# Kernel tuning notes

Hardware: AMD Instinct MI355X
Metric: run time of the kernel (lower is better)

## Reference

```python
import jax, jax.numpy as jnp
import numpy as np

B, C, H, W = 4, 320, 32, 32
HEADS = 8
LTXT, DCROSS = 77, 768
HW = H * W


def _ln(x, w, b, eps=1e-5):
    mu = x.mean(-1, keepdims=True)
    var = jnp.var(x, axis=-1, keepdims=True)
    return (x - mu) * jax.lax.rsqrt(var + eps) * w + b


def _gn(x, w, b, groups=32, eps=1e-6):
    Bx, Cx, Hx, Wx = x.shape
    xg = x.reshape(Bx, groups, -1)
    mu = xg.mean(-1, keepdims=True)
    var = jnp.var(xg, axis=-1, keepdims=True)
    xn = ((xg - mu) * jax.lax.rsqrt(var + eps)).reshape(Bx, Cx, Hx, Wx)
    return xn * w[None, :, None, None] + b[None, :, None, None]


def _attn(q, k, v, bias=None):
    Bq, S, Cd = q.shape
    dh = Cd // HEADS
    qh = q.reshape(Bq, S, HEADS, dh)
    kh = k.reshape(Bq, -1, HEADS, dh)
    vh = v.reshape(Bq, -1, HEADS, dh)
    s = jnp.einsum('bqhd,bkhd->bhqk', qh, kh) * (1.0 / np.sqrt(dh))
    if bias is not None:
        s = s + bias  # additive 0/1 otsu mask, exactly as the torch code passes it
    p = jax.nn.softmax(s, axis=-1)
    o = jnp.einsum('bhqk,bkhd->bqhd', p, vh).reshape(Bq, S, Cd)
    return o, p


def _block(x, ctx, prm, bias=None):
    # BasicTransformerBlock: self-attn -> cross-attn (returns probs) -> GEGLU FF
    (ln1w, ln1b, qkv, ow, ob, ln2w, ln2b, q2, kv2, o2w, o2b,
     ln3w, ln3b, ff1w, ff1b, ff2w, ff2b) = prm
    h = _ln(x, ln1w, ln1b)
    q, k, v = jnp.split(h @ qkv, 3, axis=-1)
    o, _ = _attn(q, k, v)
    x = x + o @ ow + ob
    h = _ln(x, ln2w, ln2b)
    k2, v2 = jnp.split(ctx @ kv2, 2, axis=-1)
    o2, p2 = _attn(h @ q2, k2, v2, bias)
    x = x + o2 @ o2w + o2b
    h = _ln(x, ln3w, ln3b)
    a, g = jnp.split(h @ ff1w + ff1b, 2, axis=-1)
    x = x + (a * jax.nn.gelu(g)) @ ff2w + ff2b
    return x, p2


def _otsu(m):
    # vectorized version of the 10-threshold otsu loop (m: [B/2, N])
    mn = m.min(-1, keepdims=True)
    mx = m.max(-1, keepdims=True)
    x = (m - mn) / (mx - mn)
    n = x.shape[-1]
    ts = jnp.arange(10, dtype=x.dtype) * 0.1  # thresholds t*0.1
    low = x[:, None, :] < ts[None, :, None]   # [B/2, 10, N]
    cnt_low = low.sum(-1).astype(x.dtype)
    cnt_high = n - cnt_low
    sum_low = jnp.where(low, x[:, None, :], 0.0).sum(-1)
    sum_high = x.sum(-1, keepdims=True) - sum_low
    mu_low = jnp.where(cnt_low > 0, sum_low / jnp.maximum(cnt_low, 1.0), jnp.nan)
    mu_high = jnp.where(cnt_high > 0, sum_high / jnp.maximum(cnt_high, 1.0), jnp.nan)
    g = (cnt_low / n) * (cnt_high / n) * (mu_low - mu_high) ** 2
    g = jnp.where(jnp.isnan(g), -jnp.inf, g)  # torch: nan > max_g is False -> skipped
    best = jnp.argmax(g, axis=-1)             # first max == torch strict-> ties keep earliest
    gmax = jnp.take_along_axis(g, best[:, None], axis=-1)[:, 0]
    thr = jnp.where(gmax > 0, best.astype(x.dtype) * 0.1, 0.0)[:, None]
    return jnp.where(x < thr, 0.0, jnp.where(x > thr, 1.0, x))


def _fwd(gn_w, gn_b, pin_w, pin_b,
         b_ln1w, b_ln1b, b_qkv, b_ow, b_ob, b_ln2w, b_ln2b, b_q2, b_kv2, b_o2w, b_o2b,
         b_ln3w, b_ln3b, b_ff1w, b_ff1b, b_ff2w, b_ff2b,
         i_ln1w, i_ln1b, i_qkv, i_ow, i_ob, i_ln2w, i_ln2b, i_q2, i_kv2, i_o2w, i_o2b,
         i_ln3w, i_ln3b, i_ff1w, i_ff1b, i_ff2w, i_ff2b,
         pout_w, pout_b, hidden_states, encoder_hidden_states,
         ph_b, ph_t, eot_b, eot_t):
    residual = hidden_states
    h = _gn(hidden_states, gn_w, gn_b)
    h = h.transpose(0, 2, 3, 1).reshape(B, HW, C)
    h = h @ pin_w + pin_b  # use_linear_projection path
    blk = (b_ln1w, b_ln1b, b_qkv, b_ow, b_ob, b_ln2w, b_ln2b, b_q2, b_kv2, b_o2w, b_o2b,
           b_ln3w, b_ln3b, b_ff1w, b_ff1b, b_ff2w, b_ff2b)
    iblk = (i_ln1w, i_ln1b, i_qkv, i_ow, i_ob, i_ln2w, i_ln2b, i_q2, i_kv2, i_o2w, i_o2b,
            i_ln3w, i_ln3b, i_ff1w, i_ff1b, i_ff2w, i_ff2b)
    h, probs = _block(h, encoder_hidden_states, blk)   # probs [B, heads, HW, 77]
    ap = probs.mean(1)[B // 2:]                        # head-avg attn_probs, cond half
    attn = ap.transpose(0, 2, 1)                       # [B/2, 77, HW]
    attn_ph = attn[ph_b, ph_t]                         # [B/2, HW]
    attn_eot = jax.lax.stop_gradient(attn[eot_b, eot_t])
    loss_reg = jnp.mean((attn_ph / attn_ph.max(-1, keepdims=True)
                         - attn_eot / attn_eot.max(-1, keepdims=True)) ** 2)
    mask = _otsu(jax.lax.stop_gradient(attn_ph))       # [B/2, HW]
    bias = mask[:, None, None, :]                      # broadcast over heads and queries
    hs, img = h[:B // 2], h[B // 2:]
    hs, _ = _block(hs, img, iblk, bias)                # image_cross_attention
    h = jnp.concatenate([hs, img], axis=0)
    h = h @ pout_w + pout_b
    sample = h.reshape(B, H, W, C).transpose(0, 3, 1, 2) + residual
    return sample, loss_reg


def setup_inputs():
    key = jax.random.key(0)
    ki = iter(jax.random.split(key, 80))
    f32 = jnp.float32

    def rn(shape, s=0.02):
        return jax.random.normal(next(ki), shape, f32) * s

    def blk(p, cross):
        return {p + 'ln1w': jnp.ones((C,), f32), p + 'ln1b': jnp.zeros((C,), f32),
                p + 'qkv': rn((C, 3 * C)), p + 'ow': rn((C, C)), p + 'ob': jnp.zeros((C,), f32),
                p + 'ln2w': jnp.ones((C,), f32), p + 'ln2b': jnp.zeros((C,), f32),
                p + 'q2': rn((C, C)), p + 'kv2': rn((cross, 2 * C)),
                p + 'o2w': rn((C, C)), p + 'o2b': jnp.zeros((C,), f32),
                p + 'ln3w': jnp.ones((C,), f32), p + 'ln3b': jnp.zeros((C,), f32),
                p + 'ff1w': rn((C, 8 * C)), p + 'ff1b': jnp.zeros((8 * C,), f32),
                p + 'ff2w': rn((4 * C, C)), p + 'ff2b': jnp.zeros((C,), f32)}

    inp = {'gn_w': jnp.ones((C,), f32), 'gn_b': jnp.zeros((C,), f32),
           'pin_w': rn((C, C)), 'pin_b': jnp.zeros((C,), f32)}
    inp.update(blk('b_', DCROSS))
    inp.update(blk('i_', C))
    inp['pout_w'] = rn((C, C))
    inp['pout_b'] = jnp.zeros((C,), f32)
    inp['hidden_states'] = jax.random.normal(next(ki), (B, C, H, W), f32)
    inp['encoder_hidden_states'] = jax.random.normal(next(ki), (B, LTXT, DCROSS), f32)
    inp['ph_b'] = jnp.arange(B // 2)
    inp['ph_t'] = jax.random.randint(next(ki), (B // 2,), 0, LTXT)
    inp['eot_b'] = jnp.arange(B // 2)
    inp['eot_t'] = jax.random.randint(next(ki), (B // 2,), 0, LTXT)
    return inp


def reference(gn_w, gn_b, pin_w, pin_b,
              b_ln1w, b_ln1b, b_qkv, b_ow, b_ob, b_ln2w, b_ln2b, b_q2, b_kv2, b_o2w, b_o2b,
              b_ln3w, b_ln3b, b_ff1w, b_ff1b, b_ff2w, b_ff2b,
              i_ln1w, i_ln1b, i_qkv, i_ow, i_ob, i_ln2w, i_ln2b, i_q2, i_kv2, i_o2w, i_o2b,
              i_ln3w, i_ln3b, i_ff1w, i_ff1b, i_ff2w, i_ff2b,
              pout_w, pout_b, hidden_states, encoder_hidden_states,
              ph_b, ph_t, eot_b, eot_t):
    return _fwd(gn_w, gn_b, pin_w, pin_b,
                b_ln1w, b_ln1b, b_qkv, b_ow, b_ob, b_ln2w, b_ln2b, b_q2, b_kv2, b_o2w, b_o2b,
                b_ln3w, b_ln3b, b_ff1w, b_ff1b, b_ff2w, b_ff2b,
                i_ln1w, i_ln1b, i_qkv, i_ow, i_ob, i_ln2w, i_ln2b, i_q2, i_kv2, i_o2w, i_o2b,
                i_ln3w, i_ln3b, i_ff1w, i_ff1b, i_ff2w, i_ff2b,
                pout_w, pout_b, hidden_states, encoder_hidden_states,
                ph_b, ph_t, eot_b, eot_t)
```

## Files before the change

kernel.cpp:

```cpp
#include <hip/hip_runtime.h>
#include <hip/hip_bf16.h>
#include <math.h>

#define NH 8
#define DH 40
#define CCH 320
#define SCALE 0.15811388300841897f

typedef __attribute__((ext_vector_type(8))) short short8;
typedef __attribute__((ext_vector_type(4))) float float4v;

static __device__ __forceinline__ unsigned short f2bf(float x) {
  __hip_bfloat16 t = __float2bfloat16(x);
  return *reinterpret_cast<unsigned short*>(&t);
}

static __device__ __forceinline__ void gload16(const void* g, void* l) {
  __builtin_amdgcn_global_load_lds((__attribute__((address_space(1))) void*)g,
                                   (__attribute__((address_space(3))) void*)l, 16, 0, 0);
}

__global__ __launch_bounds__(256) void gn_kernel(const float* __restrict__ x,
                                                 const float* __restrict__ w,
                                                 const float* __restrict__ b,
                                                 unsigned short* __restrict__ out) {
  int batch = blockIdx.x >> 5;
  int g = blockIdx.x & 31;
  const int CPG = 10;
  const float* xp = x + ((size_t)batch * CCH + g * CPG) * 1024;
  float s = 0.f, ss = 0.f;
  for (int i = threadIdx.x; i < CPG * 1024; i += 256) { float v = xp[i]; s += v; ss += v * v; }
  __shared__ float r1[256], r2[256];
  r1[threadIdx.x] = s; r2[threadIdx.x] = ss; __syncthreads();
  for (int off = 128; off > 0; off >>= 1) {
    if (threadIdx.x < off) { r1[threadIdx.x] += r1[threadIdx.x + off]; r2[threadIdx.x] += r2[threadIdx.x + off]; }
    __syncthreads();
  }
  float mu = r1[0] * (1.f / 10240.f);
  float var = r2[0] * (1.f / 10240.f) - mu * mu;
  float inv = rsqrtf(var + 1e-6f);
  for (int i = threadIdx.x; i < CPG * 1024; i += 256) {
    int ci = i >> 10; int hw = i & 1023; int c = g * CPG + ci;
    float v = (xp[i] - mu) * inv * w[c] + b[c];
    out[((size_t)batch * 1024 + hw) * CCH + c] = f2bf(v);
  }
}

__global__ __launch_bounds__(256) void ln_kernel(const float* __restrict__ x,
                                                 const float* __restrict__ w,
                                                 const float* __restrict__ b,
                                                 unsigned short* __restrict__ out, int M) {
  int row = blockIdx.x * 4 + (threadIdx.x >> 6);
  if (row >= M) return;
  const float* xp = x + (size_t)row * CCH;
  int lane = threadIdx.x & 63;
  float v[5]; float s = 0.f;
#pragma unroll
  for (int i = 0; i < 5; i++) { v[i] = xp[lane + 64 * i]; s += v[i]; }
#pragma unroll
  for (int o = 32; o > 0; o >>= 1) s += __shfl_xor(s, o);
  float mu = s * (1.f / 320.f);
  float ss = 0.f;
#pragma unroll
  for (int i = 0; i < 5; i++) { float d = v[i] - mu; ss += d * d; }
#pragma unroll
  for (int o = 32; o > 0; o >>= 1) ss += __shfl_xor(ss, o);
  float inv = rsqrtf(ss * (1.f / 320.f) + 1e-5f);
  unsigned short* op = out + (size_t)row * CCH;
#pragma unroll
  for (int i = 0; i < 5; i++) { int c = lane + 64 * i; op[c] = f2bf((v[i] - mu) * inv * w[c] + b[c]); }
}

struct WTab {
  const float* src[16];
  unsigned short* dst[16];
  int Kd[16];
  int Nd[16];
  int perm[16];
  int tstart[17];
  float* lz;
};
__global__ __launch_bounds__(256) void wconv_kernel(WTab t) {
  __shared__ float tile[32][33];
  if (blockIdx.x == 0 && threadIdx.x == 0) *t.lz = 0.f;
  int gid = blockIdx.x;
  int w = 0;
  while (w < 15 && gid >= t.tstart[w + 1]) w++;
  int local = gid - t.tstart[w];
  int K = t.Kd[w], N = t.Nd[w];
  int ntx = (N + 31) >> 5;
  int bx = local % ntx, by = local / ntx;
  int nb = bx * 32, kb = by * 32;
  const float* src = t.src[w];
  unsigned short* dst = t.dst[w];
  int doperm = t.perm[w];
  int half = N >> 1;
  int tx = threadIdx.x & 31, ty = threadIdx.x >> 5;
  for (int i = ty; i < 32; i += 8) {
    int k = kb + i, n = nb + tx;
    tile[i][tx] = (k < K && n < N) ? src[(size_t)k * N + n] : 0.f;
  }
  __syncthreads();
  for (int i = ty; i < 32; i += 8) {
    int n = nb + i, k = kb + tx;
    if (n < N && k < K) {
      int nd = n;
      if (doperm) {
        if (n < half) nd = (n >> 5) * 64 + (n & 31);
        else { int c = n - half; nd = (c >> 5) * 64 + 32 + (c & 31); }
      }
      dst[(size_t)nd * K + k] = f2bf(tile[tx][i]);
    }
  }
}

__global__ __launch_bounds__(256) void mgemm_kernel(const unsigned short* __restrict__ A,
                                                    const unsigned short* __restrict__ Bt,
                                                    const float* __restrict__ bias,
                                                    const float* __restrict__ res,
                                                    void* __restrict__ outp,
                                                    int M, int N, int K, int obf, int gl) {
  __shared__ unsigned short As[128][32];
  __shared__ unsigned short Bs[128][32];
  int tid = threadIdx.x;
  int lane = tid & 63;
  int wave = tid >> 6;
  int wm = (wave & 1) * 64;
  int wn = (wave >> 1) * 64;
  int m0 = blockIdx.y * 128;
  int n0 = blockIdx.x * 128;
  float4v acc[4][4];
  float4v zero = {0.f, 0.f, 0.f, 0.f};
#pragma unroll
  for (int i = 0; i < 4; i++)
#pragma unroll
    for (int j = 0; j < 4; j++) acc[i][j] = zero;
  int fr = lane & 15;
  int kq = (lane >> 4) * 8;
  int c0 = wave * 64 + lane;
  int c1 = c0 + 256;
  const unsigned short* a0 = A + (size_t)(m0 + (c0 >> 2)) * K + (c0 & 3) * 8;
  const unsigned short* a1 = A + (size_t)(m0 + (c1 >> 2)) * K + (c1 & 3) * 8;
  const unsigned short* b0 = Bt + (size_t)(n0 + (c0 >> 2)) * K + (c0 & 3) * 8;
  const unsigned short* b1 = Bt + (size_t)(n0 + (c1 >> 2)) * K + (c1 & 3) * 8;
  char* la0 = ((char*)As) + wave * 1024;
  char* la1 = ((char*)As) + 4096 + wave * 1024;
  char* lb0 = ((char*)Bs) + wave * 1024;
  char* lb1 = ((char*)Bs) + 4096 + wave * 1024;
  for (int k0 = 0; k0 < K; k0 += 32) {
    gload16(a0 + k0, la0);
    gload16(a1 + k0, la1);
    gload16(b0 + k0, lb0);
    gload16(b1 + k0, lb1);
    __syncthreads();
    short8 af[4], bfr[4];
#pragma unroll
    for (int i = 0; i < 4; i++) af[i] = *(short8*)&As[wm + i * 16 + fr][kq];
#pragma unroll
    for (int j = 0; j < 4; j++) bfr[j] = *(short8*)&Bs[wn + j * 16 + fr][kq];
#pragma unroll
    for (int i = 0; i < 4; i++)
#pragma unroll
      for (int j = 0; j < 4; j++)
        acc[i][j] = __builtin_amdgcn_mfma_f32_16x16x32_bf16(af[i], bfr[j], acc[i][j], 0, 0, 0);
    __syncthreads();
  }
  if (gl) {
    int half = N >> 1;
#pragma unroll
    for (int i = 0; i < 4; i++) {
      int mbase = m0 + wm + i * 16 + (lane >> 4) * 4;
#pragma unroll
      for (int jb = 0; jb < 2; jb++) {
        int nout = ((n0 + wn) >> 1) + jb * 16 + (lane & 15);
        float ba = bias[nout];
        float bg = bias[half + nout];
#pragma unroll
        for (int r = 0; r < 4; r++) {
          int m = mbase + r;
          if (m < M) {
            float a = acc[i][jb][r] + ba;
            float g = acc[i][jb + 2][r] + bg;
            float t = tanhf(0.7978845608028654f * (g + 0.044715f * g * g * g));
            ((unsigned short*)outp)[(size_t)m * half + nout] = f2bf(a * (0.5f * g * (1.f + t)));
          }
        }
      }
    }
    return;
  }
#pragma unroll
  for (int i = 0; i < 4; i++) {
    int mbase = m0 + wm + i * 16 + (lane >> 4) * 4;
#pragma unroll
    for (int j = 0; j < 4; j++) {
      int n = n0 + wn + j * 16 + (lane & 15);
      if (n >= N) continue;
      float bv = bias ? bias[n] : 0.f;
#pragma unroll
      for (int r = 0; r < 4; r++) {
        int m = mbase + r;
        if (m < M) {
          float v = acc[i][j][r] + bv;
          if (res) v += res[(size_t)m * N + n];
          if (obf) ((unsigned short*)outp)[(size_t)m * N + n] = f2bf(v);
          else ((float*)outp)[(size_t)m * N + n] = v;
        }
      }
    }
  }
}

__global__ __launch_bounds__(256) void mgemm64_kernel(const void* __restrict__ Ap,
                                                      const unsigned short* __restrict__ Bt,
                                                      const float* __restrict__ bias,
                                                      const float* __restrict__ res,
                                                      void* __restrict__ outp,
                                                      int M, int N, int K, int a32, int omode) {
  __shared__ unsigned short As[64][160];
  __shared__ unsigned short Bs[64][160];
  int tid = threadIdx.x;
  int lane = tid & 63;
  int wv = tid >> 6;
  int quad = lane >> 4;
  int col = lane & 15;
  int m0 = blockIdx.y * 64;
  int n0 = blockIdx.x * 64;
  float4v acc[4];
  float4v zero = {0.f, 0.f, 0.f, 0.f};
#pragma unroll
  for (int j = 0; j < 4; j++) acc[j] = zero;
  short8 vzero = {0, 0, 0, 0, 0, 0, 0, 0};
  int kfast = (!a32) && ((K % 160) == 0);
  int off[5];
#pragma unroll
  for (int i = 0; i < 5; i++) { int c = i * 256 + tid; int row = c / 20; off[i] = row * K + (c - row * 20) * 8; }
  int wb = (tid & 192) * 16;
  const unsigned short* Ab = (const unsigned short*)Ap + (size_t)m0 * K;
  const unsigned short* Bb = Bt + (size_t)n0 * K;
  for (int k0 = 0; k0 < K; k0 += 160) {
    if (kfast) {
#pragma unroll
      for (int i = 0; i < 5; i++) {
        gload16(Ab + off[i] + k0, ((char*)As) + wb + i * 4096);
        gload16(Bb + off[i] + k0, ((char*)Bs) + wb + i * 4096);
      }
    } else {
#pragma unroll
      for (int i = 0; i < 5; i++) {
        int u = tid + i * 256;
        int row = u / 20, seg = u - row * 20;
        int k = k0 + seg * 8;
        int m = m0 + row;
        short8 av = vzero;
        if (m < M && k < K) {
          if (a32) {
            const float* Af = (const float*)Ap;
            float4 f0 = *(const float4*)(Af + (size_t)m * K + k);
            float4 f1 = *(const float4*)(Af + (size_t)m * K + k + 4);
            av[0] = (short)f2bf(f0.x); av[1] = (short)f2bf(f0.y);
            av[2] = (short)f2bf(f0.z); av[3] = (short)f2bf(f0.w);
            av[4] = (short)f2bf(f1.x); av[5] = (short)f2bf(f1.y);
            av[6] = (short)f2bf(f1.z); av[7] = (short)f2bf(f1.w);
          } else {
            av = *(const short8*)((const unsigned short*)Ap + (size_t)m * K + k);
          }
        }
        *(short8*)&As[row][seg * 8] = av;
        int n = n0 + row;
        short8 bv = vzero;
        if (n < N && k < K) bv = *(const short8*)(Bt + (size_t)n * K + k);
        *(short8*)&Bs[row][seg * 8] = bv;
      }
    }
    __syncthreads();
#pragma unroll
    for (int kk = 0; kk < 5; kk++) {
      int kq2 = kk * 32 + quad * 8;
      short8 af = *(short8*)&As[wv * 16 + col][kq2];
#pragma unroll
      for (int j = 0; j < 4; j++) {
        short8 bfr = *(short8*)&Bs[j * 16 + col][kq2];
        acc[j] = __builtin_amdgcn_mfma_f32_16x16x32_bf16(af, bfr, acc[j], 0, 0, 0);
      }
    }
    __syncthreads();
  }
#pragma unroll
  for (int j = 0; j < 4; j++) {
    int n = n0 + j * 16 + col;
    if (n >= N) continue;
    float bv = bias ? bias[n] : 0.f;
#pragma unroll
    for (int r = 0; r < 4; r++) {
      int m = m0 + wv * 16 + quad * 4 + r;
      if (m < M) {
        float v = acc[j][r] + bv;
        if (omode == 2) {
          int bq = m >> 10, hw = m & 1023;
          size_t oi = ((size_t)bq * N + n) * 1024 + hw;
          ((float*)outp)[oi] = v + res[oi];
        } else {
          if (res) v += res[(size_t)m * N + n];
          if (omode == 1) ((unsigned short*)outp)[(size_t)m * N + n] = f2bf(v);
          else ((float*)outp)[(size_t)m * N + n] = v;
        }
      }
    }
  }
}

#define VSTR 72
__global__ __launch_bounds__(256) void mfattns_kernel(const unsigned short* __restrict__ qp, int qstr,
                                                      const unsigned short* __restrict__ kp, int kstr,
                                                      const unsigned short* __restrict__ vp, int vstr,
                                                      const float* __restrict__ bias,
                                                      float* __restrict__ Opart,
                                                      float* __restrict__ mpart,
                                                      float* __restrict__ lpart) {
  __shared__ unsigned short Ks[64 * 56];
  __shared__ unsigned short Vt[48 * VSTR];
  __shared__ unsigned short Ps[4][16 * 72];
  int tid = threadIdx.x;
  int lane = tid & 63;
  int wv = tid >> 6;
  int quad = lane >> 4;
  int col = lane & 15;
  int bid = blockIdx.x;
  int split = bid & 3;
  int qt = (bid >> 2) & 15;
  int h = (bid >> 6) & 7;
  int b = bid >> 9;

  short8 zero8 = {0, 0, 0, 0, 0, 0, 0, 0};
  int qrow = qt * 64 + wv * 16 + col;
  const unsigned short* qbase = qp + (size_t)(b * 1024 + qrow) * qstr + h * DH;
  short8 qf0 = *(const short8*)(qbase + quad * 8);
  short8 qf1 = (quad == 0) ? *(const short8*)(qbase + 32) : zero8;

  float4v Oacc[3];
  float4v fzero = {0.f, 0.f, 0.f, 0.f};
  Oacc[0] = fzero; Oacc[1] = fzero; Oacc[2] = fzero;
  float mr[4] = {-3.4e38f, -3.4e38f, -3.4e38f, -3.4e38f};
  float lr[4] = {0.f, 0.f, 0.f, 0.f};

  for (int kt = split * 4; kt < split * 4 + 4; kt++) {
    int kb = kt * 64;
    __syncthreads();
    for (int u = tid; u < 384; u += 256) {
      int key = u / 6, s = u - key * 6;
      short8 kv8 = zero8;
      if (s < 5) kv8 = *(const short8*)(kp + (size_t)(b * 1024 + kb + key) * kstr + h * DH + s * 8);
      *(short8*)&Ks[key * 56 + s * 8] = kv8;
    }
    for (int u = tid; u < 384; u += 256) {
      int s = u >> 6, key = u & 63;
      short8 vv8 = zero8;
      if (s < 5) vv8 = *(const short8*)(vp + (size_t)(b * 1024 + kb + key) * vstr + h * DH + s * 8);
#pragma unroll
      for (int j = 0; j < 8; j++) Vt[(s * 8 + j) * VSTR + key] = (unsigned short)vv8[j];
    }
    __syncthreads();

    float4v sf[4];
#pragma unroll
    for (int jb = 0; jb < 4; jb++) {
      const unsigned short* krow = &Ks[(jb * 16 + col) * 56];
      short8 bk0 = *(const short8*)(krow + quad * 8);
      short8 bk1 = (quad == 0) ? *(const short8*)(krow + 32) : zero8;
      float4v s = fzero;
      s = __builtin_amdgcn_mfma_f32_16x16x32_bf16(qf0, bk0, s, 0, 0, 0);
      s = __builtin_amdgcn_mfma_f32_16x16x32_bf16(qf1, bk1, s, 0, 0, 0);
      float bv = bias ? bias[b * 1024 + kb + jb * 16 + col] : 0.f;
#pragma unroll
      for (int r = 0; r < 4; r++) s[r] = s[r] * SCALE + bv;
      sf[jb] = s;
    }
    float tmax[4];
#pragma unroll
    for (int r = 0; r < 4; r++) {
      float t = fmaxf(fmaxf(sf[0][r], sf[1][r]), fmaxf(sf[2][r], sf[3][r]));
#pragma unroll
      for (int o = 1; o < 16; o <<= 1) t = fmaxf(t, __shfl_xor(t, o));
      tmax[r] = t;
    }
    float al[4];
#pragma unroll
    for (int r = 0; r < 4; r++) {
      float mnew = fmaxf(mr[r], tmax[r]);
      al[r] = __expf(mr[r] - mnew);
      mr[r] = mnew;
      lr[r] *= al[r];
    }
#pragma unroll
    for (int nb = 0; nb < 3; nb++)
#pragma unroll
      for (int r = 0; r < 4; r++) Oacc[nb][r] *= al[r];
    float rs[4] = {0.f, 0.f, 0.f, 0.f};
#pragma unroll
    for (int jb = 0; jb < 4; jb++) {
#pragma unroll
      for (int r = 0; r < 4; r++) {
        float p = __expf(sf[jb][r] - mr[r]);
        rs[r] += p;
        Ps[wv][(quad * 4 + r) * 72 + jb * 16 + col] = f2bf(p);
      }
    }
#pragma unroll
    for (int r = 0; r < 4; r++) {
      float t = rs[r];
#pragma unroll
      for (int o = 1; o < 16; o <<= 1) t += __shfl_xor(t, o);
      lr[r] += t;
    }
#pragma unroll
    for (int kc = 0; kc < 2; kc++) {
      int koff = kc * 32 + quad * 8;
      short8 pa = *(const short8*)&Ps[wv][col * 72 + koff];
#pragma unroll
      for (int nb = 0; nb < 3; nb++) {
        short8 vb = *(const short8*)&Vt[(nb * 16 + col) * VSTR + koff];
        Oacc[nb] = __builtin_amdgcn_mfma_f32_16x16x32_bf16(pa, vb, Oacc[nb], 0, 0, 0);
      }
    }
  }
#pragma unroll
  for (int r = 0; r < 4; r++) {
    int qo = qt * 64 + wv * 16 + quad * 4 + r;
    size_t rowidx = (size_t)(b * NH + h) * 1024 + qo;
    float* orow = Opart + (rowidx * 4 + split) * DH;
#pragma unroll
    for (int nb = 0; nb < 3; nb++) {
      int d = nb * 16 + col;
      if (d < DH) orow[d] = Oacc[nb][r];
    }
    if (col == 0) {
      mpart[rowidx * 4 + split] = mr[r];
      lpart[rowidx * 4 + split] = lr[r];
    }
  }
}

__global__ __launch_bounds__(256) void merge_kernel(const float* __restrict__ Opart,
                                                    const float* __restrict__ mpart,
                                                    const float* __restrict__ lpart,
                                                    unsigned short* __restrict__ op, int rows) {
  int r = blockIdx.x * 256 + threadIdx.x;
  if (r >= rows) return;
  float m0 = mpart[r * 4 + 0], m1 = mpart[r * 4 + 1], m2 = mpart[r * 4 + 2], m3 = mpart[r * 4 + 3];
  float M = fmaxf(fmaxf(m0, m1), fmaxf(m2, m3));
  float w0 = __expf(m0 - M), w1 = __expf(m1 - M), w2 = __expf(m2 - M), w3 = __expf(m3 - M);
  float L = lpart[r * 4 + 0] * w0 + lpart[r * 4 + 1] * w1 + lpart[r * 4 + 2] * w2 + lpart[r * 4 + 3] * w3;
  float inv = 1.f / L;
  w0 *= inv; w1 *= inv; w2 *= inv; w3 *= inv;
  int q = r & 1023;
  int h = (r >> 10) & 7;
  int b = r >> 13;
  const float4* p0 = (const float4*)(Opart + (size_t)(r * 4 + 0) * DH);
  const float4* p1 = (const float4*)(Opart + (size_t)(r * 4 + 1) * DH);
  const float4* p2 = (const float4*)(Opart + (size_t)(r * 4 + 2) * DH);
  const float4* p3 = (const float4*)(Opart + (size_t)(r * 4 + 3) * DH);
  unsigned short* o = op + ((size_t)(b * 1024 + q)) * 320 + h * DH;
#pragma unroll
  for (int j = 0; j < 10; j++) {
    float4 a = p0[j], bb = p1[j], c = p2[j], d = p3[j];
    ushort4 pk;
    pk.x = f2bf(a.x * w0 + bb.x * w1 + c.x * w2 + d.x * w3);
    pk.y = f2bf(a.y * w0 + bb.y * w1 + c.y * w2 + d.y * w3);
    pk.z = f2bf(a.z * w0 + bb.z * w1 + c.z * w2 + d.z * w3);
    pk.w = f2bf(a.w * w0 + bb.w * w1 + c.w * w2 + d.w * w3);
    *(ushort4*)(o + j * 4) = pk;
  }
}

#define CVSTR 104
__global__ __launch_bounds__(256) void cattnm_kernel(const unsigned short* __restrict__ qp,
                                                     const unsigned short* __restrict__ kvp,
                                                     unsigned short* __restrict__ op,
                                                     float* __restrict__ probs) {
  __shared__ unsigned short Ks[80 * 56];
  __shared__ unsigned short Vt[48 * CVSTR];
  __shared__ unsigned short Ps[4][16 * 104];
  int tid = threadIdx.x;
  int lane = tid & 63;
  int wv = tid >> 6;
  int quad = lane >> 4;
  int col = lane & 15;
  int bid = blockIdx.x;
  int qt = bid & 15;
  int h = (bid >> 4) & 7;
  int b = bid >> 7;

  short8 zero8 = {0, 0, 0, 0, 0, 0, 0, 0};
  for (int u = tid; u < 480; u += 256) {
    int key = u / 6, s = u - key * 6;
    short8 v8 = zero8;
    if (s < 5 && key < 77) v8 = *(const short8*)(kvp + (size_t)(b * 77 + key) * 640 + h * DH + s * 8);
    *(short8*)&Ks[key * 56 + s * 8] = v8;
  }
  for (int u = tid; u < 576; u += 256) {
    int s = u / 96, key = u - s * 96;
    short8 v8 = zero8;
    if (s < 5 && key < 77) v8 = *(const short8*)(kvp + (size_t)(b * 77 + key) * 640 + 320 + h * DH + s * 8);
#pragma unroll
    for (int j = 0; j < 8; j++) Vt[(s * 8 + j) * CVSTR + key] = (unsigned short)v8[j];
  }
  int qrow = qt * 64 + wv * 16 + col;
  const unsigned short* qbase = qp + (size_t)(b * 1024 + qrow) * CCH + h * DH;
  short8 qf0 = *(const short8*)(qbase + quad * 8);
  short8 qf1 = (quad == 0) ? *(const short8*)(qbase + 32) : zero8;
  __syncthreads();

  float4v fzero = {0.f, 0.f, 0.f, 0.f};
  float4v sf[5];
#pragma unroll
  for (int jb = 0; jb < 5; jb++) {
    const unsigned short* krow = &Ks[(jb * 16 + col) * 56];
    short8 bk0 = *(const short8*)(krow + quad * 8);
    short8 bk1 = (quad == 0) ? *(const short8*)(krow + 32) : zero8;
    float4v s = fzero;
    s = __builtin_amdgcn_mfma_f32_16x16x32_bf16(qf0, bk0, s, 0, 0, 0);
    s = __builtin_amdgcn_mfma_f32_16x16x32_bf16(qf1, bk1, s, 0, 0, 0);
    int key = jb * 16 + col;
    float msk = (key < 77) ? 0.f : -3.4e38f;
#pragma unroll
    for (int r = 0; r < 4; r++) s[r] = s[r] * SCALE + msk;
    sf[jb] = s;
  }
  float inv[4];
#pragma unroll
  for (int r = 0; r < 4; r++) {
    float t = sf[0][r];
#pragma unroll
    for (int jb = 1; jb < 5; jb++) t = fmaxf(t, sf[jb][r]);
#pragma unroll
    for (int o = 1; o < 16; o <<= 1) t = fmaxf(t, __shfl_xor(t, o));
    float sum = 0.f;
#pragma unroll
    for (int jb = 0; jb < 5; jb++) { float e = __expf(sf[jb][r] - t); sf[jb][r] = e; sum += e; }
#pragma unroll
    for (int o = 1; o < 16; o <<= 1) sum += __shfl_xor(sum, o);
    inv[r] = 1.f / sum;
  }
#pragma unroll
  for (int jb = 0; jb < 5; jb++) {
    int key = jb * 16 + col;
    float4v pv;
#pragma unroll
    for (int r = 0; r < 4; r++) {
      float p = sf[jb][r] * inv[r];
      Ps[wv][(quad * 4 + r) * 104 + jb * 16 + col] = f2bf(p);
      pv[r] = p;
    }
    if (b >= 2 && key < 77) {
      size_t pi = ((size_t)((b - 2) * NH + h) * 77 + key) * 1024 + qt * 64 + wv * 16 + quad * 4;
      *(float4v*)&probs[pi] = pv;
    }
  }
  float4v Oacc[3];
  Oacc[0] = fzero; Oacc[1] = fzero; Oacc[2] = fzero;
#pragma unroll
  for (int kc = 0; kc < 3; kc++) {
    int koff = kc * 32 + quad * 8;
    short8 pa = (koff < 80) ? *(const short8*)&Ps[wv][col * 104 + koff] : zero8;
#pragma unroll
    for (int nb = 0; nb < 3; nb++) {
      short8 vb = *(const short8*)&Vt[(nb * 16 + col) * CVSTR + koff];
      Oacc[nb] = __builtin_amdgcn_mfma_f32_16x16x32_bf16(pa, vb, Oacc[nb], 0, 0, 0);
    }
  }
#pragma unroll
  for (int r = 0; r < 4; r++) {
    int qo = qt * 64 + wv * 16 + quad * 4 + r;
    unsigned short* orow = op + (size_t)(b * 1024 + qo) * CCH + h * DH;
#pragma unroll
    for (int nb = 0; nb < 3; nb++) {
      int d = nb * 16 + col;
      if (d < DH) orow[d] = f2bf(Oacc[nb][r]);
    }
  }
}

__global__ __launch_bounds__(256) void eol_kernel(const float* __restrict__ pT,
                                                  const int* __restrict__ phb, const int* __restrict__ pht,
                                                  const int* __restrict__ eob, const int* __restrict__ eot,
                                                  float* __restrict__ mask,
                                                  float* __restrict__ lossout) {
  __shared__ float S[4][24];
  __shared__ float shthr;
  int i = blockIdx.x, tid = threadIdx.x;
  int lane = tid & 63, wv = tid >> 6;
  int pb = phb[i], pt = pht[i], eb = eob[i], et = eot[i];
  float x[4], y[4];
#pragma unroll
  for (int j = 0; j < 4; j++) {
    int q = tid + 256 * j;
    float s1 = 0.f, s2 = 0.f;
#pragma unroll
    for (int hh = 0; hh < NH; hh++) {
      s1 += pT[((size_t)(pb * NH + hh) * 77 + pt) * 1024 + q];
      s2 += pT[((size_t)(eb * NH + hh) * 77 + et) * 1024 + q];
    }
    x[j] = s1 * 0.125f;
    y[j] = s2 * 0.125f;
  }
  float mx = fmaxf(fmaxf(x[0], x[1]), fmaxf(x[2], x[3]));
  float me = fmaxf(fmaxf(y[0], y[1]), fmaxf(y[2], y[3]));
  float mn = fminf(fminf(x[0], x[1]), fminf(x[2], x[3]));
  float sx = x[0] + x[1] + x[2] + x[3];
#pragma unroll
  for (int o = 32; o > 0; o >>= 1) {
    mx = fmaxf(mx, __shfl_xor(mx, o));
    me = fmaxf(me, __shfl_xor(me, o));
    mn = fminf(mn, __shfl_xor(mn, o));
    sx += __shfl_xor(sx, o);
  }
  if (lane == 0) { S[wv][0] = mx; S[wv][1] = me; S[wv][2] = mn; S[wv][3] = sx; }
  __syncthreads();
  mx = fmaxf(fmaxf(S[0][0], S[1][0]), fmaxf(S[2][0], S[3][0]));
  me = fmaxf(fmaxf(S[0][1], S[1][1]), fmaxf(S[2][1], S[3][1]));
  mn = fminf(fminf(S[0][2], S[1][2]), fminf(S[2][2], S[3][2]));
  sx = S[0][3] + S[1][3] + S[2][3] + S[3][3];
  float invmp = 1.f / mx, invme = 1.f / me;
  float inv = 1.f / (mx - mn);
  float lp = 0.f;
  float cnt[10], sm[10];
#pragma unroll
  for (int t = 0; t < 10; t++) { cnt[t] = 0.f; sm[t] = 0.f; }
#pragma unroll
  for (int j = 0; j < 4; j++) {
    float d = x[j] * invmp - y[j] * invme;
    lp += d * d;
    float v = (x[j] - mn) * inv;
#pragma unroll
    for (int t = 0; t < 10; t++) {
      if (v < t * 0.1f) { cnt[t] += 1.f; sm[t] += v; }
    }
  }
#pragma unroll
  for (int o = 32; o > 0; o >>= 1) {
    lp += __shfl_xor(lp, o);
#pragma unroll
    for (int t = 0; t < 10; t++) { cnt[t] += __shfl_xor(cnt[t], o); sm[t] += __shfl_xor(sm[t], o); }
  }
  __syncthreads();
  if (lane == 0) {
    S[wv][0] = lp;
#pragma unroll
    for (int t = 0; t < 10; t++) { S[wv][1 + t] = cnt[t]; S[wv][11 + t] = sm[t]; }
  }
  __syncthreads();
  if (tid == 0) {
    float lpt = S[0][0] + S[1][0] + S[2][0] + S[3][0];
    atomicAdd(lossout, lpt * (1.f / 2048.f));
    float total = (sx - 1024.f * mn) * inv;
    float gmax = -3.4e38f; int best = 0;
    for (int t = 0; t < 10; t++) {
      float c_low = S[0][1 + t] + S[1][1 + t] + S[2][1 + t] + S[3][1 + t];
      float s_low = S[0][11 + t] + S[1][11 + t] + S[2][11 + t] + S[3][11 + t];
      float c_high = 1024.f - c_low;
      float g;
      if (c_low > 0.f && c_high > 0.f) {
        float mu_l = s_low / c_low;
        float mu_h = (total - s_low) / c_high;
        float dd = mu_l - mu_h;
        g = (c_low * (1.f / 1024.f)) * (c_high * (1.f / 1024.f)) * dd * dd;
      } else g = -3.4e38f;
      if (g > gmax) { gmax = g; best = t; }
    }
    shthr = (gmax > 0.f) ? best * 0.1f : 0.f;
  }
  __syncthreads();
  float thr = shthr;
#pragma unroll
  for (int j = 0; j < 4; j++) {
    int q = tid + 256 * j;
    float v = (x[j] - mn) * inv;
    mask[i * 1024 + q] = (v < thr) ? 0.f : ((v > thr) ? 1.f : v);
  }
}

extern "C" void kernel_launch(void* const* d_in, const int* in_sizes, int n_in,
                              void* d_out, int out_size, void* d_ws, size_t ws_size,
                              hipStream_t stream) {
  auto F = [&](int i) { return (const float*)d_in[i]; };
  auto I = [&](int i) { return (const int*)d_in[i]; };

  float* ws = (float*)d_ws;
  float* h    = ws;
  float* ffb  = h    + 1310720;
  float* p2   = ffb  + 10485760;
  float* mask = p2   + 2523136;

  float* Opart = ffb;
  float* mpart = ffb + 5242880;
  float* lpart = ffb + 5242880 + 131072;

  unsigned short* b16   = (unsigned short*)(mask + 2048);
  unsigned short* lnb16 = b16;
  unsigned short* attb16= lnb16 + 1310720;
  unsigned short* actb16= attb16 + 1310720;
  unsigned short* qkv16 = actb16 + 5242880;
  unsigned short* q16   = qkv16 + 3932160;
  unsigned short* kv16  = q16 + 1310720;
  unsigned short* wptr  = kv16 + 1310720;

  auto walloc = [&](int n) { unsigned short* p = wptr; wptr += n; return p; };
  unsigned short* pin_t  = walloc(102400);
  unsigned short* bqkv_t = walloc(307200);
  unsigned short* bow_t  = walloc(102400);
  unsigned short* bq2_t  = walloc(102400);
  unsigned short* bkv2_t = walloc(491520);
  unsigned short* bo2_t  = walloc(102400);
  unsigned short* bff1_t = walloc(819200);
  unsigned short* bff2_t = walloc(409600);
  unsigned short* iqkv_t = walloc(307200);
  unsigned short* iow_t  = walloc(102400);
  unsigned short* iq2_t  = walloc(102400);
  unsigned short* ikv2_t = walloc(204800);
  unsigned short* io2_t  = walloc(102400);
  unsigned short* iff1_t = walloc(819200);
  unsigned short* iff2_t = walloc(409600);
  unsigned short* pout_t = walloc(102400);

  float* out = (float*)d_out;

  WTab wt;
  wt.lz = out + 1310720;
  int nt = 0, cnt = 0;
  auto addw = [&](const float* s, unsigned short* d, int K, int N, int perm) {
    wt.src[cnt] = s; wt.dst[cnt] = d; wt.Kd[cnt] = K; wt.Nd[cnt] = N; wt.perm[cnt] = perm;
    wt.tstart[cnt] = nt;
    nt += ((K + 31) / 32) * ((N + 31) / 32);
    cnt++;
  };
  addw(F(2), pin_t, 320, 320, 0);
  addw(F(4 + 2), bqkv_t, 320, 960, 0);
  addw(F(4 + 3), bow_t, 320, 320, 0);
  addw(F(4 + 7), bq2_t, 320, 320, 0);
  addw(F(4 + 8), bkv2_t, 768, 640, 0);
  addw(F(4 + 9), bo2_t, 320, 320, 0);
  addw(F(4 + 13), bff1_t, 320, 2560, 1);
  addw(F(4 + 15), bff2_t, 1280, 320, 0);
  addw(F(21 + 2), iqkv_t, 320, 960, 0);
  addw(F(21 + 3), iow_t, 320, 320, 0);
  addw(F(21 + 7), iq2_t, 320, 320, 0);
  addw(F(21 + 8), ikv2_t, 320, 640, 0);
  addw(F(21 + 9), io2_t, 320, 320, 0);
  addw(F(21 + 13), iff1_t, 320, 2560, 1);
  addw(F(21 + 15), iff2_t, 1280, 320, 0);
  addw(F(38), pout_t, 320, 320, 0);
  wt.tstart[16] = nt;

  wconv_kernel<<<nt, 256, 0, stream>>>(wt);

  auto gemm64 = [&](const void* A, const unsigned short* Wt, const float* bias,
                    const float* res, void* o, int M, int N, int K, int a32, int omode) {
    dim3 g((N + 63) / 64, (M + 63) / 64);
    mgemm64_kernel<<<g, 256, 0, stream>>>(A, Wt, bias, res, o, M, N, K, a32, omode);
  };
  auto gemm128 = [&](const unsigned short* A, const unsigned short* Wt, const float* bias,
                     const float* res, void* o, int M, int N, int K, int obf, int gl) {
    dim3 g((N + 127) / 128, (M + 127) / 128);
    mgemm_kernel<<<g, 256, 0, stream>>>(A, Wt, bias, res, o, M, N, K, obf, gl);
  };

  gn_kernel<<<128, 256, 0, stream>>>(F(40), F(0), F(1), lnb16);
  gemm64(lnb16, pin_t, F(3), nullptr, h, 4096, 320, 320, 0, 0);

  auto run_block = [&](int p, int Bx, bool img_block,
                       const unsigned short* qkv_t, const unsigned short* ow_t,
                       const unsigned short* q2_t, const unsigned short* kv2_t,
                       const unsigned short* o2_t, const unsigned short* ff1_t,
                       const unsigned short* ff2_t) {
    int M = Bx * 1024;
    ln_kernel<<<M / 4, 256, 0, stream>>>(h, F(p + 0), F(p + 1), lnb16, M);
    gemm128(lnb16, qkv_t, nullptr, nullptr, qkv16, M, 960, 320, 1, 0);
    mfattns_kernel<<<Bx * 512, 256, 0, stream>>>(qkv16, 960, qkv16 + 320, 960, qkv16 + 640, 960,
                                                 nullptr, Opart, mpart, lpart);
    merge_kernel<<<Bx * 32, 256, 0, stream>>>(Opart, mpart, lpart, attb16, Bx * 8192);
    gemm64(attb16, ow_t, F(p + 4), h, h, M, 320, 320, 0, 0);
    ln_kernel<<<M / 4, 256, 0, stream>>>(h, F(p + 5), F(p + 6), lnb16, M);
    if (!img_block) {
      gemm64(F(41), kv2_t, nullptr, nullptr, kv16, Bx * 77, 640, 768, 1, 1);
      gemm64(lnb16, q2_t, nullptr, nullptr, q16, M, 320, 320, 0, 1);
      cattnm_kernel<<<Bx * 128, 256, 0, stream>>>(q16, kv16, attb16, p2);
    } else {
      gemm64(h + (size_t)2 * 1024 * 320, kv2_t, nullptr, nullptr, kv16, Bx * 1024, 640, 320, 1, 1);
      gemm64(lnb16, q2_t, nullptr, nullptr, q16, M, 320, 320, 0, 1);
      mfattns_kernel<<<Bx * 512, 256, 0, stream>>>(q16, 320, kv16, 640, kv16 + 320, 640,
                                                   mask, Opart, mpart, lpart);
      merge_kernel<<<Bx * 32, 256, 0, stream>>>(Opart, mpart, lpart, attb16, Bx * 8192);
    }
    gemm64(attb16, o2_t, F(p + 10), h, h, M, 320, 320, 0, 0);
    ln_kernel<<<M / 4, 256, 0, stream>>>(h, F(p + 11), F(p + 12), lnb16, M);
    gemm128(lnb16, ff1_t, F(p + 14), nullptr, actb16, M, 2560, 320, 1, 1);
    gemm64(actb16, ff2_t, F(p + 16), h, h, M, 320, 1280, 0, 0);
  };

  run_block(4, 4, false, bqkv_t, bow_t, bq2_t, bkv2_t, bo2_t, bff1_t, bff2_t);

  eol_kernel<<<2, 256, 0, stream>>>(p2, I(42), I(43), I(44), I(45), mask, out + 1310720);

  run_block(21, 2, true, iqkv_t, iow_t, iq2_t, ikv2_t, io2_t, iff1_t, iff2_t);

  gemm64(h, pout_t, F(39), F(40), out, 4096, 320, 320, 1, 2);
}
```

Before: 579.3 us.

## Fuse LayerNorm into GEMM prologues and attention merge into output projection

Removes the standalone LayerNorm and split-attention merge kernels. LayerNorm is now computed inside new GEMM kernels that normalize a full 128- or 64-row K=320 A tile into shared memory before the MFMA loop, which double-buffers the weight tiles. The merge of partial attention outputs now runs in the prologue of a 64x64 output-projection GEMM that adds the residual in place. This cuts kernel launches and round trips of bf16 intermediates through global memory. In exchange, each N-tile block recomputes LayerNorm or the merge for its rows, shared-memory use per block rises sharply, and the M-bounds checks are dropped.

```diff
diff --git a/kernel.cpp b/kernel.cpp
--- a/kernel.cpp
+++ b/kernel.cpp
@@ -44,31 +44,6 @@
     float v = (xp[i] - mu) * inv * w[c] + b[c];
     out[((size_t)batch * 1024 + hw) * CCH + c] = f2bf(v);
   }
-}
-
-__global__ __launch_bounds__(256) void ln_kernel(const float* __restrict__ x,
-                                                 const float* __restrict__ w,
-                                                 const float* __restrict__ b,
-                                                 unsigned short* __restrict__ out, int M) {
-  int row = blockIdx.x * 4 + (threadIdx.x >> 6);
-  if (row >= M) return;
-  const float* xp = x + (size_t)row * CCH;
-  int lane = threadIdx.x & 63;
-  float v[5]; float s = 0.f;
-#pragma unroll
-  for (int i = 0; i < 5; i++) { v[i] = xp[lane + 64 * i]; s += v[i]; }
-#pragma unroll
-  for (int o = 32; o > 0; o >>= 1) s += __shfl_xor(s, o);
-  float mu = s * (1.f / 320.f);
-  float ss = 0.f;
-#pragma unroll
-  for (int i = 0; i < 5; i++) { float d = v[i] - mu; ss += d * d; }
-#pragma unroll
-  for (int o = 32; o > 0; o >>= 1) ss += __shfl_xor(ss, o);
-  float inv = rsqrtf(ss * (1.f / 320.f) + 1e-5f);
-  unsigned short* op = out + (size_t)row * CCH;
-#pragma unroll
-  for (int i = 0; i < 5; i++) { int c = lane + 64 * i; op[c] = f2bf((v[i] - mu) * inv * w[c] + b[c]); }
 }
 
 struct WTab {
@@ -114,50 +89,84 @@
   }
 }
 
-__global__ __launch_bounds__(256) void mgemm_kernel(const unsigned short* __restrict__ A,
-                                                    const unsigned short* __restrict__ Bt,
-                                                    const float* __restrict__ bias,
-                                                    const float* __restrict__ res,
-                                                    void* __restrict__ outp,
-                                                    int M, int N, int K, int obf, int gl) {
-  __shared__ unsigned short As[128][32];
-  __shared__ unsigned short Bs[128][32];
+__global__ __launch_bounds__(256) void lngemm128_kernel(const float* __restrict__ A,
+                                                        const float* __restrict__ lnw,
+                                                        const float* __restrict__ lnb,
+                                                        const unsigned short* __restrict__ Bt,
+                                                        const float* __restrict__ bias,
+                                                        unsigned short* __restrict__ outp,
+                                                        int M, int N, int gl) {
+  __shared__ unsigned short As[128][328];
+  __shared__ unsigned short Bsd[2][128][32];
+  __shared__ float Wf[320], Bf[320];
+  __shared__ float Mu[128], Iv[128];
+  const int K = 320;
   int tid = threadIdx.x;
   int lane = tid & 63;
   int wave = tid >> 6;
+  int m0 = blockIdx.y * 128;
+  int n0 = blockIdx.x * 128;
+  int c0 = wave * 64 + lane;
+  int c1 = c0 + 256;
+  const unsigned short* bp0 = Bt + (size_t)(n0 + (c0 >> 2)) * K + (c0 & 3) * 8;
+  const unsigned short* bp1 = Bt + (size_t)(n0 + (c1 >> 2)) * K + (c1 & 3) * 8;
+  gload16(bp0, ((char*)Bsd[0]) + wave * 1024);
+  gload16(bp1, ((char*)Bsd[0]) + 4096 + wave * 1024);
+  for (int i = tid; i < 320; i += 256) { Wf[i] = lnw[i]; Bf[i] = lnb[i]; }
+  int l32 = tid & 31;
+  int rsub = tid >> 5;
+  for (int it = 0; it < 16; it++) {
+    int r = it * 8 + rsub;
+    const float* ap = A + (size_t)(m0 + r) * K;
+    float s = 0.f, ss = 0.f;
+#pragma unroll
+    for (int j = 0; j < 10; j++) { float v = ap[l32 + j * 32]; s += v; ss += v * v; }
+#pragma unroll
+    for (int o = 16; o > 0; o >>= 1) { s += __shfl_xor(s, o); ss += __shfl_xor(ss, o); }
+    if (l32 == 0) {
+      float mu = s * (1.f / 320.f);
+      Mu[r] = mu;
+      Iv[r] = rsqrtf(ss * (1.f / 320.f) - mu * mu + 1e-5f);
+    }
+  }
+  __syncthreads();
+#pragma unroll 4
+  for (int i = 0; i < 40; i++) {
+    int cc = i * 256 + tid;
+    int r = cc / 80, c4 = cc - r * 80;
+    int col = c4 * 4;
+    float4 v = *(const float4*)(A + (size_t)(m0 + r) * K + col);
+    float mu = Mu[r], iv = Iv[r];
+    ushort4 o;
+    o.x = f2bf((v.x - mu) * iv * Wf[col] + Bf[col]);
+    o.y = f2bf((v.y - mu) * iv * Wf[col + 1] + Bf[col + 1]);
+    o.z = f2bf((v.z - mu) * iv * Wf[col + 2] + Bf[col + 2]);
+    o.w = f2bf((v.w - mu) * iv * Wf[col + 3] + Bf[col + 3]);
+    *(ushort4*)&As[r][col] = o;
+  }
+  __syncthreads();
   int wm = (wave & 1) * 64;
   int wn = (wave >> 1) * 64;
-  int m0 = blockIdx.y * 128;
-  int n0 = blockIdx.x * 128;
+  int fr = lane & 15;
+  int kq = (lane >> 4) * 8;
   float4v acc[4][4];
   float4v zero = {0.f, 0.f, 0.f, 0.f};
 #pragma unroll
   for (int i = 0; i < 4; i++)
 #pragma unroll
     for (int j = 0; j < 4; j++) acc[i][j] = zero;
-  int fr = lane & 15;
-  int kq = (lane >> 4) * 8;
-  int c0 = wave * 64 + lane;
-  int c1 = c0 + 256;
-  const unsigned short* a0 = A + (size_t)(m0 + (c0 >> 2)) * K + (c0 & 3) * 8;
-  const unsigned short* a1 = A + (size_t)(m0 + (c1 >> 2)) * K + (c1 & 3) * 8;
-  const unsigned short* b0 = Bt + (size_t)(n0 + (c0 >> 2)) * K + (c0 & 3) * 8;
-  const unsigned short* b1 = Bt + (size_t)(n0 + (c1 >> 2)) * K + (c1 & 3) * 8;
-  char* la0 = ((char*)As) + wave * 1024;
-  char* la1 = ((char*)As) + 4096 + wave * 1024;
-  char* lb0 = ((char*)Bs) + wave * 1024;
-  char* lb1 = ((char*)Bs) + 4096 + wave * 1024;
-  for (int k0 = 0; k0 < K; k0 += 32) {
-    gload16(a0 + k0, la0);
-    gload16(a1 + k0, la1);
-    gload16(b0 + k0, lb0);
-    gload16(b1 + k0, lb1);
-    __syncthreads();
+  for (int t = 0; t < 10; t++) {
+    if (t < 9) {
+      int kn = (t + 1) * 32;
+      gload16(bp0 + kn, ((char*)Bsd[(t + 1) & 1]) + wave * 1024);
+      gload16(bp1 + kn, ((char*)Bsd[(t + 1) & 1]) + 4096 + wave * 1024);
+    }
+    int k0 = t * 32;
     short8 af[4], bfr[4];
 #pragma unroll
-    for (int i = 0; i < 4; i++) af[i] = *(short8*)&As[wm + i * 16 + fr][kq];
-#pragma unroll
-    for (int j = 0; j < 4; j++) bfr[j] = *(short8*)&Bs[wn + j * 16 + fr][kq];
+    for (int i = 0; i < 4; i++) af[i] = *(short8*)&As[wm + i * 16 + fr][k0 + kq];
+#pragma unroll
+    for (int j = 0; j < 4; j++) bfr[j] = *(short8*)&Bsd[t & 1][wn + j * 16 + fr][kq];
 #pragma unroll
     for (int i = 0; i < 4; i++)
 #pragma unroll
@@ -178,12 +187,10 @@
 #pragma unroll
         for (int r = 0; r < 4; r++) {
           int m = mbase + r;
-          if (m < M) {
-            float a = acc[i][jb][r] + ba;
-            float g = acc[i][jb + 2][r] + bg;
-            float t = tanhf(0.7978845608028654f * (g + 0.044715f * g * g * g));
-            ((unsigned short*)outp)[(size_t)m * half + nout] = f2bf(a * (0.5f * g * (1.f + t)));
-          }
+          float a = acc[i][jb][r] + ba;
+          float g = acc[i][jb + 2][r] + bg;
+          float t2 = tanhf(0.7978845608028654f * (g + 0.044715f * g * g * g));
+          outp[(size_t)m * half + nout] = f2bf(a * (0.5f * g * (1.f + t2)));
         }
       }
     }
@@ -200,13 +207,167 @@
 #pragma unroll
       for (int r = 0; r < 4; r++) {
         int m = mbase + r;
-        if (m < M) {
-          float v = acc[i][j][r] + bv;
-          if (res) v += res[(size_t)m * N + n];
-          if (obf) ((unsigned short*)outp)[(size_t)m * N + n] = f2bf(v);
-          else ((float*)outp)[(size_t)m * N + n] = v;
-        }
+        outp[(size_t)m * N + n] = f2bf(acc[i][j][r] + bv);
       }
+    }
+  }
+}
+
+__global__ __launch_bounds__(256) void lngemm64_kernel(const float* __restrict__ A,
+                                                       const float* __restrict__ lnw,
+                                                       const float* __restrict__ lnb,
+                                                       const unsigned short* __restrict__ Bt,
+                                                       unsigned short* __restrict__ outp,
+                                                       int M, int N) {
+  __shared__ unsigned short As[64][328];
+  __shared__ unsigned short Bsd[2][64][32];
+  __shared__ float Wf[320], Bf[320];
+  __shared__ float Mu[64], Iv[64];
+  const int K = 320;
+  int tid = threadIdx.x;
+  int lane = tid & 63;
+  int wv = tid >> 6;
+  int quad = lane >> 4;
+  int col = lane & 15;
+  int m0 = blockIdx.y * 64;
+  int n0 = blockIdx.x * 64;
+  const unsigned short* bp0 = Bt + (size_t)(n0 + (tid >> 2)) * K + (tid & 3) * 8;
+  gload16(bp0, ((char*)Bsd[0]) + wv * 1024);
+  for (int i = tid; i < 320; i += 256) { Wf[i] = lnw[i]; Bf[i] = lnb[i]; }
+  int l32 = tid & 31;
+  int rsub = tid >> 5;
+  for (int it = 0; it < 8; it++) {
+    int r = it * 8 + rsub;
+    const float* ap = A + (size_t)(m0 + r) * K;
+    float s = 0.f, ss = 0.f;
+#pragma unroll
+    for (int j = 0; j < 10; j++) { float v = ap[l32 + j * 32]; s += v; ss += v * v; }
+#pragma unroll
+    for (int o = 16; o > 0; o >>= 1) { s += __shfl_xor(s, o); ss += __shfl_xor(ss, o); }
+    if (l32 == 0) {
+      float mu = s * (1.f / 320.f);
+      Mu[r] = mu;
+      Iv[r] = rsqrtf(ss * (1.f / 320.f) - mu * mu + 1e-5f);
+    }
+  }
+  __syncthreads();
+#pragma unroll 4
+  for (int i = 0; i < 20; i++) {
+    int cc = i * 256 + tid;
+    int r = cc / 80, c4 = cc - r * 80;
+    int c = c4 * 4;
+    float4 v = *(const float4*)(A + (size_t)(m0 + r) * K + c);
+    float mu = Mu[r], iv = Iv[r];
+    ushort4 o;
+    o.x = f2bf((v.x - mu) * iv * Wf[c] + Bf[c]);
+    o.y = f2bf((v.y - mu) * iv * Wf[c + 1] + Bf[c + 1]);
+    o.z = f2bf((v.z - mu) * iv * Wf[c + 2] + Bf[c + 2]);
+    o.w = f2bf((v.w - mu) * iv * Wf[c + 3] + Bf[c + 3]);
+    *(ushort4*)&As[r][c] = o;
+  }
+  __syncthreads();
+  float4v acc[4];
+  float4v zero = {0.f, 0.f, 0.f, 0.f};
+#pragma unroll
+  for (int j = 0; j < 4; j++) acc[j] = zero;
+  for (int t = 0; t < 10; t++) {
+    if (t < 9) gload16(bp0 + (t + 1) * 32, ((char*)Bsd[(t + 1) & 1]) + wv * 1024);
+    int k0 = t * 32;
+    short8 af = *(short8*)&As[wv * 16 + col][k0 + quad * 8];
+#pragma unroll
+    for (int j = 0; j < 4; j++) {
+      short8 bfr = *(short8*)&Bsd[t & 1][j * 16 + col][quad * 8];
+      acc[j] = __builtin_amdgcn_mfma_f32_16x16x32_bf16(af, bfr, acc[j], 0, 0, 0);
+    }
+    __syncthreads();
+  }
+#pragma unroll
+  for (int j = 0; j < 4; j++) {
+    int n = n0 + j * 16 + col;
+#pragma unroll
+    for (int r = 0; r < 4; r++) {
+      int m = m0 + wv * 16 + quad * 4 + r;
+      outp[(size_t)m * N + n] = f2bf(acc[j][r]);
+    }
+  }
+}
+
+__global__ __launch_bounds__(256) void mergegemm64_kernel(const float* __restrict__ Opart,
+                                                          const float* __restrict__ mpart,
+                                                          const float* __restrict__ lpart,
+                                                          const unsigned short* __restrict__ Bt,
+                                                          const float* __restrict__ bias,
+                                                          float* __restrict__ h, int M) {
+  __shared__ unsigned short As[64][328];
+  __shared__ unsigned short Bsd[2][64][32];
+  const int K = 320;
+  int tid = threadIdx.x;
+  int lane = tid & 63;
+  int wv = tid >> 6;
+  int quad = lane >> 4;
+  int col = lane & 15;
+  int m0 = blockIdx.y * 64;
+  int n0 = blockIdx.x * 64;
+  const unsigned short* bp0 = Bt + (size_t)(n0 + (tid >> 2)) * K + (tid & 3) * 8;
+  gload16(bp0, ((char*)Bsd[0]) + wv * 1024);
+#pragma unroll
+  for (int i = 0; i < 10; i++) {
+    int cc = i * 256 + tid;
+    int r = cc / 40, c8 = cc - r * 40;
+    int c = c8 * 8;
+    int hh = c / 40;
+    int d = c - hh * 40;
+    int m = m0 + r, b = m >> 10, q = m & 1023;
+    size_t ri = ((size_t)(b * NH + hh) * 1024 + q) * 4;
+    float ma = mpart[ri], mb = mpart[ri + 1], mc = mpart[ri + 2], md = mpart[ri + 3];
+    float Mx = fmaxf(fmaxf(ma, mb), fmaxf(mc, md));
+    float w0 = __expf(ma - Mx), w1 = __expf(mb - Mx), w2 = __expf(mc - Mx), w3 = __expf(md - Mx);
+    float L = lpart[ri] * w0 + lpart[ri + 1] * w1 + lpart[ri + 2] * w2 + lpart[ri + 3] * w3;
+    float inv = 1.f / L;
+    w0 *= inv; w1 *= inv; w2 *= inv; w3 *= inv;
+    const float* p0 = Opart + (ri + 0) * DH + d;
+    const float* p1 = Opart + (ri + 1) * DH + d;
+    const float* p2 = Opart + (ri + 2) * DH + d;
+    const float* p3 = Opart + (ri + 3) * DH + d;
+    float4 a0 = *(const float4*)p0, a1 = *(const float4*)p1, a2 = *(const float4*)p2, a3 = *(const float4*)p3;
+    float4 b0 = *(const float4*)(p0 + 4), b1 = *(const float4*)(p1 + 4), b2 = *(const float4*)(p2 + 4), b3 = *(const float4*)(p3 + 4);
+    ushort4 u0, u1;
+    u0.x = f2bf(a0.x * w0 + a1.x * w1 + a2.x * w2 + a3.x * w3);
+    u0.y = f2bf(a0.y * w0 + a1.y * w1 + a2.y * w2 + a3.y * w3);
+    u0.z = f2bf(a0.z * w0 + a1.z * w1 + a2.z * w2 + a3.z * w3);
+    u0.w = f2bf(a0.w * w0 + a1.w * w1 + a2.w * w2 + a3.w * w3);
+    u1.x = f2bf(b0.x * w0 + b1.x * w1 + b2.x * w2 + b3.x * w3);
+    u1.y = f2bf(b0.y * w0 + b1.y * w1 + b2.y * w2 + b3.y * w3);
+    u1.z = f2bf(b0.z * w0 + b1.z * w1 + b2.z * w2 + b3.z * w3);
+    u1.w = f2bf(b0.w * w0 + b1.w * w1 + b2.w * w2 + b3.w * w3);
+    *(ushort4*)&As[r][c] = u0;
+    *(ushort4*)&As[r][c + 4] = u1;
+  }
+  __syncthreads();
+  float4v acc[4];
+  float4v zero = {0.f, 0.f, 0.f, 0.f};
+#pragma unroll
+  for (int j = 0; j < 4; j++) acc[j] = zero;
+  for (int t = 0; t < 10; t++) {
+    if (t < 9) gload16(bp0 + (t + 1) * 32, ((char*)Bsd[(t + 1) & 1]) + wv * 1024);
+    int k0 = t * 32;
+    short8 af = *(short8*)&As[wv * 16 + col][k0 + quad * 8];
+#pragma unroll
+    for (int j = 0; j < 4; j++) {
+      short8 bfr = *(short8*)&Bsd[t & 1][j * 16 + col][quad * 8];
+      acc[j] = __builtin_amdgcn_mfma_f32_16x16x32_bf16(af, bfr, acc[j], 0, 0, 0);
+    }
+    __syncthreads();
+  }
+#pragma unroll
+  for (int j = 0; j < 4; j++) {
+    int n = n0 + j * 16 + col;
+    float bv = bias[n];
+#pragma unroll
+    for (int r = 0; r < 4; r++) {
+      int m = m0 + wv * 16 + quad * 4 + r;
+      size_t oi = (size_t)m * 320 + n;
+      h[oi] = acc[j][r] + bv + h[oi];
     }
   }
 }
@@ -438,38 +599,6 @@
       mpart[rowidx * 4 + split] = mr[r];
       lpart[rowidx * 4 + split] = lr[r];
     }
-  }
-}
-
-__global__ __launch_bounds__(256) void merge_kernel(const float* __restrict__ Opart,
-                                                    const float* __restrict__ mpart,
-                                                    const float* __restrict__ lpart,
-                                                    unsigned short* __restrict__ op, int rows) {
-  int r = blockIdx.x * 256 + threadIdx.x;
-  if (r >= rows) return;
-  float m0 = mpart[r * 4 + 0], m1 = mpart[r * 4 + 1], m2 = mpart[r * 4 + 2], m3 = mpart[r * 4 + 3];
-  float M = fmaxf(fmaxf(m0, m1), fmaxf(m2, m3));
-  float w0 = __expf(m0 - M), w1 = __expf(m1 - M), w2 = __expf(m2 - M), w3 = __expf(m3 - M);
-  float L = lpart[r * 4 + 0] * w0 + lpart[r * 4 + 1] * w1 + lpart[r * 4 + 2] * w2 + lpart[r * 4 + 3] * w3;
-  float inv = 1.f / L;
-  w0 *= inv; w1 *= inv; w2 *= inv; w3 *= inv;
-  int q = r & 1023;
-  int h = (r >> 10) & 7;
-  int b = r >> 13;
-  const float4* p0 = (const float4*)(Opart + (size_t)(r * 4 + 0) * DH);
-  const float4* p1 = (const float4*)(Opart + (size_t)(r * 4 + 1) * DH);
-  const float4* p2 = (const float4*)(Opart + (size_t)(r * 4 + 2) * DH);
-  const float4* p3 = (const float4*)(Opart + (size_t)(r * 4 + 3) * DH);
-  unsigned short* o = op + ((size_t)(b * 1024 + q)) * 320 + h * DH;
-#pragma unroll
-  for (int j = 0; j < 10; j++) {
-    float4 a = p0[j], bb = p1[j], c = p2[j], d = p3[j];
-    ushort4 pk;
-    pk.x = f2bf(a.x * w0 + bb.x * w1 + c.x * w2 + d.x * w3);
-    pk.y = f2bf(a.y * w0 + bb.y * w1 + c.y * w2 + d.y * w3);
-    pk.z = f2bf(a.z * w0 + bb.z * w1 + c.z * w2 + d.z * w3);
-    pk.w = f2bf(a.w * w0 + bb.w * w1 + c.w * w2 + d.w * w3);
-    *(ushort4*)(o + j * 4) = pk;
   }
 }
 
@@ -759,10 +888,20 @@
     dim3 g((N + 63) / 64, (M + 63) / 64);
     mgemm64_kernel<<<g, 256, 0, stream>>>(A, Wt, bias, res, o, M, N, K, a32, omode);
   };
-  auto gemm128 = [&](const unsigned short* A, const unsigned short* Wt, const float* bias,
-                     const float* res, void* o, int M, int N, int K, int obf, int gl) {
-    dim3 g((N + 127) / 128, (M + 127) / 128);
-    mgemm_kernel<<<g, 256, 0, stream>>>(A, Wt, bias, res, o, M, N, K, obf, gl);
+  auto lngemm128 = [&](const float* A, const float* lw, const float* lb,
+                       const unsigned short* Wt, const float* bias,
+                       unsigned short* o, int M, int N, int gl) {
+    dim3 g((N + 127) / 128, M / 128);
+    lngemm128_kernel<<<g, 256, 0, stream>>>(A, lw, lb, Wt, bias, o, M, N, gl);
+  };
+  auto lngemm64 = [&](const float* A, const float* lw, const float* lb,
+                      const unsigned short* Wt, unsigned short* o, int M, int N) {
+    dim3 g(N / 64, M / 64);
+    lngemm64_kernel<<<g, 256, 0, stream>>>(A, lw, lb, Wt, o, M, N);
+  };
+  auto mergegemm = [&](const unsigned short* Wt, const float* bias, int M) {
+    dim3 g(5, M / 64);
+    mergegemm64_kernel<<<g, 256, 0, stream>>>(Opart, mpart, lpart, Wt, bias, h, M);
   };
 
   gn_kernel<<<128, 256, 0, stream>>>(F(40), F(0), F(1), lnb16);
@@ -774,27 +913,22 @@
                        const unsigned short* o2_t, const unsigned short* ff1_t,
                        const unsigned short* ff2_t) {
     int M = Bx * 1024;
-    ln_kernel<<<M / 4, 256, 0, stream>>>(h, F(p + 0), F(p + 1), lnb16, M);
-    gemm128(lnb16, qkv_t, nullptr, nullptr, qkv16, M, 960, 320, 1, 0);
+    lngemm128(h, F(p + 0), F(p + 1), qkv_t, nullptr, qkv16, M, 960, 0);
     mfattns_kernel<<<Bx * 512, 256, 0, stream>>>(qkv16, 960, qkv16 + 320, 960, qkv16 + 640, 960,
                                                  nullptr, Opart, mpart, lpart);
-    merge_kernel<<<Bx * 32, 256, 0, stream>>>(Opart, mpart, lpart, attb16, Bx * 8192);
-    gemm64(attb16, ow_t, F(p + 4), h, h, M, 320, 320, 0, 0);
-    ln_kernel<<<M / 4, 256, 0, stream>>>(h, F(p + 5), F(p + 6), lnb16, M);
+    mergegemm(ow_t, F(p + 4), M);
+    lngemm64(h, F(p + 5), F(p + 6), q2_t, q16, M, 320);
     if (!img_block) {
       gemm64(F(41), kv2_t, nullptr, nullptr, kv16, Bx * 77, 640, 768, 1, 1);
-      gemm64(lnb16, q2_t, nullptr, nullptr, q16, M, 320, 320, 0, 1);
       cattnm_kernel<<<Bx * 128, 256, 0, stream>>>(q16, kv16, attb16, p2);
+      gemm64(attb16, o2_t, F(p + 10), h, h, M, 320, 320, 0, 0);
     } else {
       gemm64(h + (size_t)2 * 1024 * 320, kv2_t, nullptr, nullptr, kv16, Bx * 1024, 640, 320, 1, 1);
-      gemm64(lnb16, q2_t, nullptr, nullptr, q16, M, 320, 320, 0, 1);
       mfattns_kernel<<<Bx * 512, 256, 0, stream>>>(q16, 320, kv16, 640, kv16 + 320, 640,
                                                    mask, Opart, mpart, lpart);
-      merge_kernel<<<Bx * 32, 256, 0, stream>>>(Opart, mpart, lpart, attb16, Bx * 8192);
-    }
-    gemm64(attb16, o2_t, F(p + 10), h, h, M, 320, 320, 0, 0);
-    ln_kernel<<<M / 4, 256, 0, stream>>>(h, F(p + 11), F(p + 12), lnb16, M);
-    gemm128(lnb16, ff1_t, F(p + 14), nullptr, actb16, M, 2560, 320, 1, 1);
+      mergegemm(o2_t, F(p + 10), M);
+    }
+    lngemm128(h, F(p + 11), F(p + 12), ff1_t, F(p + 14), actb16, M, 2560, 1);
     gemm64(actb16, ff2_t, F(p + 16), h, h, M, 320, 1280, 0, 0);
   };
 
```

Result: slower. 628.4 us (+8.5%).
